# Kernel optimization log

Measured on AMD Instinct MI355X. Metric: run time of the kernel, lower is better.

Reference implementation:

```python
import jax, jax.numpy as jnp
import numpy as np

B, T, DIM, H = 4, 2048, 512, 8
DECAY = 0.9

def setup_inputs():
    key = jax.random.key(0)
    ks = jax.random.split(key, 8)
    s = 1.0 / np.sqrt(DIM)
    def lin(k):
        return jax.random.normal(k, (DIM, DIM), jnp.float32) * s
    return {
        "q": jax.random.normal(ks[0], (B, T, DIM), jnp.float32),
        "k": jax.random.normal(ks[1], (B, T, DIM), jnp.float32),
        "v": jax.random.normal(ks[2], (B, T, DIM), jnp.float32),
        "Wa": lin(ks[3]), "ba": jnp.zeros((DIM,), jnp.float32),
        "Wb": lin(ks[4]), "bb": jnp.zeros((DIM,), jnp.float32),
        "Wg": lin(ks[5]), "bg": jnp.zeros((DIM,), jnp.float32),
        "Wo": lin(ks[6]), "bo": jnp.zeros((DIM,), jnp.float32),
    }

def _linear_scan(a, b):
    # h_t = a_t * h_{t-1} + b_t along time axis=1, via associative scan
    def combine(c1, c2):
        a1, b1 = c1
        a2, b2 = c2
        return a1 * a2, a2 * b1 + b2
    return jax.lax.associative_scan(combine, (a, b), axis=1)[1]

def reference(q, k, v, Wa, ba, Wb, bb, Wg, bg, Wo, bo):
    # --- Mamba-style selective scan on q (no residual) ---
    a = jax.nn.sigmoid(q @ Wa + ba)   # input-dependent decay [B,T,D]
    b = q @ Wb + bb                   # input injection       [B,T,D]
    h = _linear_scan(a, b)            # recurrent state       [B,T,D]
    g = jax.nn.sigmoid(q @ Wg + bg)   # gate
    m_out = (h * g) @ Wo + bo         # [B,T,D]

    # --- RetNet-style decay-weighted linear retention ---
    Dh = DIM // H
    qh = q.reshape(B, T, H, Dh)
    kh = k.reshape(B, T, H, Dh)
    vh = v.reshape(B, T, H, Dh)
    t = jnp.arange(T)
    delta = t[:, None] - t[None, :]           # t - s
    mask = delta >= 0                         # causal
    decay_mat = jnp.where(
        mask,
        jnp.exp(jnp.where(mask, delta, 0).astype(jnp.float32) * np.float32(np.log(DECAY))),
        0.0,
    )                                          # [T,T]
    scores = jnp.einsum('bthd,bshd->bhts', qh, kh) * decay_mat  # [B,H,T,T]
    r_out = jnp.einsum('bhts,bshd->bthd', scores, vh).reshape(B, T, DIM)

    return m_out + r_out
```

## Files before the change

### kernel.cpp

```cpp
#include <hip/hip_runtime.h>
#include <hip/hip_bf16.h>

typedef unsigned short u16;

#define BB 4
#define TT 2048
#define DIM 512
#define NH 8
#define DH 64
#define DECAY 0.9f

#define CC 64
#define NC 32
#define BHN 32

#define CHS 32
#define NSC 64

#define TM 128
#define TN 128
#define BK 64

#define SS 72

typedef __attribute__((ext_vector_type(8))) short bf16x8;
typedef __attribute__((ext_vector_type(4))) float f32x4;

__device__ __forceinline__ u16 f2bfu(float f) {
  union { float f; unsigned int u; } c; c.f = f;
  unsigned int u = c.u + 0x7FFFu + ((c.u >> 16) & 1u);
  return (u16)(u >> 16);
}
__device__ __forceinline__ float bf2f(u16 u) {
  union { unsigned int u; float f; } c; c.u = ((unsigned int)u) << 16;
  return c.f;
}

__device__ __forceinline__ void gl_lds16(const void* g, void* l) {
  __builtin_amdgcn_global_load_lds(
      (const __attribute__((address_space(1))) void*)g,
      (__attribute__((address_space(3))) void*)(unsigned int)(unsigned long long)l,
      16, 0, 0);
}

__device__ __forceinline__ void gemm_tile(
    int nTile, int mTile, const u16* __restrict__ A, const u16* __restrict__ Bt,
    const float* __restrict__ b0, const float* __restrict__ b1,
    const float* __restrict__ b2,
    u16* __restrict__ C0, u16* __restrict__ C1, u16* __restrict__ C2,
    int act_mask, u16* As, u16* Bs, int tid) {
  int wave = tid >> 6, lane = tid & 63;
  int group = (nTile * TN) >> 9;
  const float* bias = (group == 0) ? b0 : (group == 1) ? b1 : b2;
  u16* C = (group == 0) ? C0 : (group == 1) ? C1 : C2;
  int act = (act_mask >> group) & 1;

  int wm = (wave >> 1) * 64, wn = (wave & 1) * 64;
  int rowA = lane & 15, khalf = lane >> 4;

  f32x4 acc[4][4];
#pragma unroll
  for (int i = 0; i < 4; ++i)
#pragma unroll
    for (int j = 0; j < 4; ++j) acc[i][j] = (f32x4){0.f, 0.f, 0.f, 0.f};

  const u16* Abase = A + (size_t)mTile * TM * 512;
  const u16* Bbase = Bt + (size_t)nTile * TN * 512;

  for (int kk = 0; kk < 512; kk += BK) {
#pragma unroll
    for (int i = 0; i < 4; ++i) {
      int o = (wave * 4 + i) * 64 + lane;
      int row = o >> 3, gk = (o & 7) ^ (row & 7);
      gl_lds16(Abase + (size_t)row * 512 + kk + gk * 8, &As[o * 8]);
    }
#pragma unroll
    for (int i = 0; i < 4; ++i) {
      int o = (wave * 4 + i) * 64 + lane;
      int row = o >> 3, gk = (o & 7) ^ (row & 7);
      gl_lds16(Bbase + (size_t)row * 512 + kk + gk * 8, &Bs[o * 8]);
    }
    __syncthreads();
#pragma unroll
    for (int k0 = 0; k0 < 2; ++k0) {
      bf16x8 af[4], bfr[4];
#pragma unroll
      for (int mi = 0; mi < 4; ++mi) {
        int rr = wm + mi * 16 + rowA;
        int gk = k0 * 4 + khalf;
        int o = rr * 8 + (gk ^ (rr & 7));
        af[mi] = *(const bf16x8*)&As[o * 8];
      }
#pragma unroll
      for (int ni = 0; ni < 4; ++ni) {
        int rr = wn + ni * 16 + rowA;
        int gk = k0 * 4 + khalf;
        int o = rr * 8 + (gk ^ (rr & 7));
        bfr[ni] = *(const bf16x8*)&Bs[o * 8];
      }
#pragma unroll
      for (int mi = 0; mi < 4; ++mi)
#pragma unroll
        for (int ni = 0; ni < 4; ++ni)
          acc[mi][ni] = __builtin_amdgcn_mfma_f32_16x16x32_bf16(
              af[mi], bfr[ni], acc[mi][ni], 0, 0, 0);
    }
    __syncthreads();
  }
  int cloc = lane & 15, rq = (lane >> 4) * 4;
#pragma unroll
  for (int mi = 0; mi < 4; ++mi) {
#pragma unroll
    for (int r = 0; r < 4; ++r) {
      int m = mTile * TM + wm + mi * 16 + rq + r;
#pragma unroll
      for (int ni = 0; ni < 4; ++ni) {
        int n = (nTile * TN + wn + ni * 16 + cloc) & 511;
        float vv = acc[mi][ni][r] + bias[n];
        if (act) vv = 1.0f / (1.0f + __expf(-vv));
        C[(size_t)m * 512 + n] = f2bfu(vv);
      }
    }
  }
}

__device__ __forceinline__ void gemm_tile64(
    int nTile, int mTile, const u16* __restrict__ A, const u16* __restrict__ Bt,
    const float* __restrict__ bias, float* __restrict__ C,
    const u16* __restrict__ Radd, u16* As, u16* Bs, int tid) {
  int wave = tid >> 6, lane = tid & 63;
  int wm = wave * 32;
  int rowA = lane & 15, khalf = lane >> 4;

  f32x4 acc[2][4];
#pragma unroll
  for (int i = 0; i < 2; ++i)
#pragma unroll
    for (int j = 0; j < 4; ++j) acc[i][j] = (f32x4){0.f, 0.f, 0.f, 0.f};

  const u16* Abase = A + (size_t)mTile * TM * 512;
  const u16* Bbase = Bt + (size_t)nTile * 64 * 512;

  for (int kk = 0; kk < 512; kk += BK) {
#pragma unroll
    for (int i = 0; i < 4; ++i) {
      int o = (wave * 4 + i) * 64 + lane;
      int row = o >> 3, gk = (o & 7) ^ (row & 7);
      gl_lds16(Abase + (size_t)row * 512 + kk + gk * 8, &As[o * 8]);
    }
#pragma unroll
    for (int i = 0; i < 2; ++i) {
      int o = (wave * 2 + i) * 64 + lane;
      int row = o >> 3, gk = (o & 7) ^ (row & 7);
      gl_lds16(Bbase + (size_t)row * 512 + kk + gk * 8, &Bs[o * 8]);
    }
    __syncthreads();
#pragma unroll
    for (int k0 = 0; k0 < 2; ++k0) {
      bf16x8 af[2], bfr[4];
#pragma unroll
      for (int mi = 0; mi < 2; ++mi) {
        int rr = wm + mi * 16 + rowA;
        int gk = k0 * 4 + khalf;
        int o = rr * 8 + (gk ^ (rr & 7));
        af[mi] = *(const bf16x8*)&As[o * 8];
      }
#pragma unroll
      for (int ni = 0; ni < 4; ++ni) {
        int rr = ni * 16 + rowA;
        int gk = k0 * 4 + khalf;
        int o = rr * 8 + (gk ^ (rr & 7));
        bfr[ni] = *(const bf16x8*)&Bs[o * 8];
      }
#pragma unroll
      for (int mi = 0; mi < 2; ++mi)
#pragma unroll
        for (int ni = 0; ni < 4; ++ni)
          acc[mi][ni] = __builtin_amdgcn_mfma_f32_16x16x32_bf16(
              af[mi], bfr[ni], acc[mi][ni], 0, 0, 0);
    }
    __syncthreads();
  }
  int cloc = lane & 15, rq = (lane >> 4) * 4;
#pragma unroll
  for (int mi = 0; mi < 2; ++mi) {
#pragma unroll
    for (int r = 0; r < 4; ++r) {
      int m = mTile * TM + wm + mi * 16 + rq + r;
#pragma unroll
      for (int ni = 0; ni < 4; ++ni) {
        int n = nTile * 64 + ni * 16 + cloc;
        float vv = acc[mi][ni][r] + bias[n] + bf2f(Radd[(size_t)m * 512 + n]);
        C[(size_t)m * 512 + n] = vv;
      }
    }
  }
}

__global__ __launch_bounds__(256) void k1_prep_retkv(
    const float* __restrict__ q, u16* __restrict__ qbf,
    const float* __restrict__ W0, const float* __restrict__ W1,
    const float* __restrict__ W2, const float* __restrict__ W3,
    u16* __restrict__ Wt,
    const float* __restrict__ k, const float* __restrict__ v,
    u16* __restrict__ KVTb, u16* __restrict__ VTg, u16* __restrict__ kcb) {
  __shared__ __align__(16) u16 smem[2 * 64 * SS];
  __shared__ float t[32][33];
  int bx = blockIdx.x, tid = threadIdx.x;
  if (bx < 1024) {
    int bh = bx & 31, c = bx >> 5;
    int b = bh >> 3, h = bh & 7;
    int wave = tid >> 6, lane = tid & 63;
    u16* VT = smem;
    u16* KT = smem + 64 * SS;
    size_t base = ((size_t)(b * TT + c * CC)) * DIM + h * DH;
    int row = tid >> 2, part = tid & 3, e0 = part * 16;
    float w = __powf(DECAY, (float)(63 - row));
    __align__(16) u16 krow[16];
    {
      const float4* vs = (const float4*)(v + base + (size_t)row * DIM + e0);
      const float4* ks = (const float4*)(k + base + (size_t)row * DIM + e0);
#pragma unroll
      for (int u4 = 0; u4 < 4; ++u4) {
        float4 fv = vs[u4], fk = ks[u4];
        VT[(e0 + u4 * 4 + 0) * SS + row] = f2bfu(fv.x);
        VT[(e0 + u4 * 4 + 1) * SS + row] = f2bfu(fv.y);
        VT[(e0 + u4 * 4 + 2) * SS + row] = f2bfu(fv.z);
        VT[(e0 + u4 * 4 + 3) * SS + row] = f2bfu(fv.w);
        u16 k0s = f2bfu(fk.x * w), k1s = f2bfu(fk.y * w);
        u16 k2s = f2bfu(fk.z * w), k3s = f2bfu(fk.w * w);
        KT[(e0 + u4 * 4 + 0) * SS + row] = k0s;
        KT[(e0 + u4 * 4 + 1) * SS + row] = k1s;
        KT[(e0 + u4 * 4 + 2) * SS + row] = k2s;
        KT[(e0 + u4 * 4 + 3) * SS + row] = k3s;
        krow[u4 * 4 + 0] = k0s; krow[u4 * 4 + 1] = k1s;
        krow[u4 * 4 + 2] = k2s; krow[u4 * 4 + 3] = k3s;
      }
    }
    {
      u16* kdst = kcb + (((size_t)bh * NC + c) * 64 + row) * 64 + e0;
      *(uint4*)kdst = *(const uint4*)&krow[0];
      *(uint4*)(kdst + 8) = *(const uint4*)&krow[8];
    }
    __syncthreads();
    {
      int e = row;
      u16* dst = VTg + ((size_t)bh * 64 + e) * TT + c * 64 + part * 16;
      *(uint4*)dst = *(const uint4*)&VT[e * SS + part * 16];
      *(uint4*)(dst + 8) = *(const uint4*)&VT[e * SS + part * 16 + 8];
    }
    int wm = (wave >> 1) * 32, wn = (wave & 1) * 32;
    int rowA = lane & 15, khalf = lane >> 4;
    f32x4 acc[2][2];
#pragma unroll
    for (int i = 0; i < 2; ++i)
#pragma unroll
      for (int j = 0; j < 2; ++j) acc[i][j] = (f32x4){0.f, 0.f, 0.f, 0.f};
#pragma unroll
    for (int k0 = 0; k0 < 2; ++k0) {
      int gk = k0 * 4 + khalf;
      bf16x8 af[2], bfr[2];
#pragma unroll
      for (int mi = 0; mi < 2; ++mi)
        af[mi] = *(const bf16x8*)&VT[(wm + mi * 16 + rowA) * SS + gk * 8];
#pragma unroll
      for (int ni = 0; ni < 2; ++ni)
        bfr[ni] = *(const bf16x8*)&KT[(wn + ni * 16 + rowA) * SS + gk * 8];
#pragma unroll
      for (int mi = 0; mi < 2; ++mi)
#pragma unroll
        for (int ni = 0; ni < 2; ++ni)
          acc[mi][ni] = __builtin_amdgcn_mfma_f32_16x16x32_bf16(
              af[mi], bfr[ni], acc[mi][ni], 0, 0, 0);
    }
    int cloc = lane & 15, rq = (lane >> 4) * 4;
    u16* o = KVTb + ((size_t)(c * BHN + bh)) * 4096;
#pragma unroll
    for (int mi = 0; mi < 2; ++mi)
#pragma unroll
      for (int r = 0; r < 4; ++r) {
        int e = wm + mi * 16 + rq + r;
#pragma unroll
        for (int ni = 0; ni < 2; ++ni)
          o[e * 64 + (wn + ni * 16 + cloc)] = f2bfu(acc[mi][ni][r]);
      }
  } else if (bx < 2048) {
    int bx2 = bx - 1024;
    int m = bx2 >> 8, rem = bx2 & 255;
    int n0 = (rem & 15) * 32, k0 = (rem >> 4) * 32;
    const float* W = (m == 0) ? W0 : (m == 1) ? W1 : (m == 2) ? W2 : W3;
    int tx = tid & 31, ty = tid >> 5;
#pragma unroll
    for (int r = 0; r < 32; r += 8)
      t[ty + r][tx] = W[(size_t)(k0 + ty + r) * DIM + n0 + tx];
    __syncthreads();
    u16* o = Wt + (size_t)m * DIM * DIM;
#pragma unroll
    for (int r = 0; r < 32; r += 8)
      o[(size_t)(n0 + ty + r) * DIM + k0 + tx] = f2bfu(t[tx][ty + r]);
  } else {
    int i = (bx - 2048) * 256 + tid;
    float4 f = ((const float4*)q)[i];
    ushort4 u;
    u.x = f2bfu(f.x); u.y = f2bfu(f.y); u.z = f2bfu(f.z); u.w = f2bfu(f.w);
    ((ushort4*)qbf)[i] = u;
  }
}

__global__ __launch_bounds__(256) void k2_gemm1_retscan(
    const u16* __restrict__ qbf, const u16* __restrict__ WtAll,
    const float* __restrict__ ba, const float* __restrict__ bb,
    const float* __restrict__ bg,
    u16* __restrict__ Ab16, u16* __restrict__ Bb16, u16* __restrict__ Gb16,
    const u16* __restrict__ KVTb, u16* __restrict__ Ptb) {
  __shared__ __align__(16) u16 smem[TM * BK + TN * BK];
  int bx = blockIdx.x, tid = threadIdx.x;
  if (bx < 768) {
    int r = bx & 7, t6 = bx >> 3;
    int nT = t6 % 12, s = t6 / 12;
    int mT = (s << 3) | r;
    gemm_tile(nT, mT, qbf, WtAll, ba, bb, bg, Ab16, Bb16, Gb16,
              0b101, smem, smem + TM * BK, tid);
  } else {
    int gid = (bx - 768) * 256 + tid;
    int bh = gid >> 12, ed = gid & 4095;
    float carry = 0.f;
    const float dC = __powf(DECAY, (float)CC);
    for (int c = 0; c < NC; ++c) {
      size_t idx = ((size_t)(c * BHN + bh)) * 4096 + ed;
      Ptb[idx] = f2bfu(carry);
      carry = fmaf(dC, carry, bf2f(KVTb[idx]));
    }
  }
}

__global__ __launch_bounds__(256) void k3_retout_part(
    const u16* __restrict__ Ab16, const u16* __restrict__ Bb16,
    float* __restrict__ SA, float* __restrict__ SB,
    const u16* __restrict__ qbf, const u16* __restrict__ kcb,
    const u16* __restrict__ VTg, const u16* __restrict__ Ptb,
    u16* __restrict__ routb) {
  __shared__ __align__(16) u16 Sa[64 * SS];
  __shared__ float dp[66];
  __shared__ float dpi[64];
  int bx = blockIdx.x, tid = threadIdx.x;
  if (bx >= 1024) {
    int bxp = bx - 1024;
    int ci = bxp >> 3, grp = bxp & 7;
    int ch = grp * 256 + tid;
    int bb2 = ch >> 9, d = ch & 511;
    size_t base = ((size_t)bb2 * TT + ci * CHS) * DIM + d;
    float h = 0.f, pA = 1.f;
#pragma unroll
    for (int t = 0; t < CHS; ++t) {
      float av = bf2f(Ab16[base + (size_t)t * DIM]);
      float bv = bf2f(Bb16[base + (size_t)t * DIM]);
      h = fmaf(av, h, bv);
      pA *= av;
    }
    SA[ci * 2048 + ch] = pA;
    SB[ci * 2048 + ch] = h;
    return;
  }
  int bh = bx & 31, c = bx >> 5;
  int b = bh >> 3, h = bh & 7;
  int wave = tid >> 6, lane = tid & 63;
  size_t base = ((size_t)(b * TT + c * CC)) * DIM + h * DH;
  if (tid < 66) dp[tid] = __powf(DECAY, (float)tid);
  if (tid < 64) dpi[tid] = __powf(DECAY, (float)tid - 63.0f);

  int wm = (wave >> 1) * 32, wn = (wave & 1) * 32;
  int rowA = lane & 15, khalf = lane >> 4;

  bf16x8 afq[2][2];
#pragma unroll
  for (int k0 = 0; k0 < 2; ++k0)
#pragma unroll
    for (int mi = 0; mi < 2; ++mi)
      afq[k0][mi] = *(const bf16x8*)(qbf + base +
          (size_t)(wm + mi * 16 + rowA) * 512 + (k0 * 4 + khalf) * 8);
  const u16* kcbase = kcb + ((size_t)bh * NC + c) * 64 * 64;
  bf16x8 bfk[2][2];
#pragma unroll
  for (int k0 = 0; k0 < 2; ++k0)
#pragma unroll
    for (int ni = 0; ni < 2; ++ni)
      bfk[k0][ni] = *(const bf16x8*)(kcbase +
          (size_t)(wn + ni * 16 + rowA) * 64 + (k0 * 4 + khalf) * 8);

  f32x4 accS[2][2];
#pragma unroll
  for (int i = 0; i < 2; ++i)
#pragma unroll
    for (int j = 0; j < 2; ++j) accS[i][j] = (f32x4){0.f, 0.f, 0.f, 0.f};
#pragma unroll
  for (int k0 = 0; k0 < 2; ++k0)
#pragma unroll
    for (int mi = 0; mi < 2; ++mi)
#pragma unroll
      for (int ni = 0; ni < 2; ++ni)
        accS[mi][ni] = __builtin_amdgcn_mfma_f32_16x16x32_bf16(
            afq[k0][mi], bfk[k0][ni], accS[mi][ni], 0, 0, 0);
  __syncthreads();

  int cloc = lane & 15, rq = (lane >> 4) * 4;
#pragma unroll
  for (int mi = 0; mi < 2; ++mi)
#pragma unroll
    for (int ni = 0; ni < 2; ++ni)
#pragma unroll
      for (int r = 0; r < 4; ++r) {
        int i = wm + mi * 16 + rq + r;
        int j = wn + ni * 16 + cloc;
        float sv = (j <= i) ? accS[mi][ni][r] * dpi[i] : 0.f;
        Sa[i * SS + j] = f2bfu(sv);
      }
#pragma unroll
  for (int mi = 0; mi < 2; ++mi) {
    float s = dp[wm + mi * 16 + rowA + 1];
#pragma unroll
    for (int k0 = 0; k0 < 2; ++k0) {
      bf16x8 t = afq[k0][mi];
#pragma unroll
      for (int u = 0; u < 8; ++u)
        t[u] = (short)f2bfu(bf2f((u16)t[u]) * s);
      afq[k0][mi] = t;
    }
  }
  __syncthreads();

  f32x4 accO[2][2];
#pragma unroll
  for (int i = 0; i < 2; ++i)
#pragma unroll
    for (int j = 0; j < 2; ++j) accO[i][j] = (f32x4){0.f, 0.f, 0.f, 0.f};
#pragma unroll
  for (int k0 = 0; k0 < 4; ++k0) {
    bf16x8 af[2], bfv[2];
#pragma unroll
    for (int mi = 0; mi < 2; ++mi) {
      if (k0 < 2)
        af[mi] = *(const bf16x8*)&Sa[(wm + mi * 16 + rowA) * SS +
                                     (k0 * 4 + khalf) * 8];
      else
        af[mi] = afq[k0 - 2][mi];
    }
#pragma unroll
    for (int ni = 0; ni < 2; ++ni) {
      int e = wn + ni * 16 + rowA;
      if (k0 < 2)
        bfv[ni] = *(const bf16x8*)(VTg + ((size_t)bh * 64 + e) * TT + c * 64 +
                                   (k0 * 4 + khalf) * 8);
      else
        bfv[ni] = *(const bf16x8*)(Ptb + ((size_t)(c * BHN + bh)) * 4096 +
                                   e * 64 + ((k0 - 2) * 4 + khalf) * 8);
    }
#pragma unroll
    for (int mi = 0; mi < 2; ++mi)
#pragma unroll
      for (int ni = 0; ni < 2; ++ni)
        accO[mi][ni] = __builtin_amdgcn_mfma_f32_16x16x32_bf16(
            af[mi], bfv[ni], accO[mi][ni], 0, 0, 0);
  }
#pragma unroll
  for (int mi = 0; mi < 2; ++mi)
#pragma unroll
    for (int r = 0; r < 4; ++r) {
      int i = wm + mi * 16 + rq + r;
#pragma unroll
      for (int ni = 0; ni < 2; ++ni) {
        int e = wn + ni * 16 + cloc;
        routb[base + (size_t)i * 512 + e] = f2bfu(accO[mi][ni][r]);
      }
    }
}

__global__ __launch_bounds__(256) void k4_apply(
    const u16* __restrict__ Ab16, const u16* __restrict__ Bb16,
    const u16* __restrict__ g, const float* __restrict__ SA,
    const float* __restrict__ SB, u16* __restrict__ hg) {
  int bx = blockIdx.x, tid = threadIdx.x;
  int ci = bx >> 3, grp = bx & 7;
  int ch = grp * 256 + tid;
  int bb = ch >> 9, d = ch & 511;
  float carry = 0.f;
  for (int p = 0; p < ci; ++p)
    carry = fmaf(SA[p * 2048 + ch], carry, SB[p * 2048 + ch]);
  size_t base = ((size_t)bb * TT + ci * CHS) * DIM + d;
  float h = carry;
#pragma unroll
  for (int t = 0; t < CHS; ++t) {
    size_t idx = base + (size_t)t * DIM;
    h = fmaf(bf2f(Ab16[idx]), h, bf2f(Bb16[idx]));
    hg[idx] = f2bfu(h * bf2f(g[idx]));
  }
}

__global__ __launch_bounds__(256) void k5_gemm2(
    const u16* __restrict__ hgbf, const u16* __restrict__ Wto,
    const float* __restrict__ bo, float* __restrict__ out,
    const u16* __restrict__ routb) {
  __shared__ __align__(16) u16 smem[TM * BK + 64 * BK];
  int bx = blockIdx.x;
  int r = bx & 7, t6 = bx >> 3;
  int nT = t6 & 7, s = t6 >> 3;
  int mT = (s << 3) | r;
  gemm_tile64(nT, mT, hgbf, Wto, bo, out, routb,
              smem, smem + TM * BK, threadIdx.x);
}

extern "C" void kernel_launch(void* const* d_in, const int* in_sizes, int n_in,
                              void* d_out, int out_size, void* d_ws, size_t ws_size,
                              hipStream_t stream) {
  const float* q  = (const float*)d_in[0];
  const float* k  = (const float*)d_in[1];
  const float* v  = (const float*)d_in[2];
  const float* Wa = (const float*)d_in[3];
  const float* ba = (const float*)d_in[4];
  const float* Wb = (const float*)d_in[5];
  const float* bb = (const float*)d_in[6];
  const float* Wg = (const float*)d_in[7];
  const float* bg = (const float*)d_in[8];
  const float* Wo = (const float*)d_in[9];
  const float* bo = (const float*)d_in[10];
  float* out = (float*)d_out;
  float* ws = (float*)d_ws;

  const size_t NEL = (size_t)BB * TT * DIM;
  float* SA = ws;
  float* SB = SA + NSC * 2048;
  u16* up = (u16*)(SB + NSC * 2048);
  u16* Ab16  = up;  up += NEL;
  u16* Bb16  = up;  up += NEL;
  u16* Gb16  = up;  up += NEL;
  u16* qbf   = up;  up += NEL;
  u16* hgbf  = up;  up += NEL;
  u16* WtAll = up;  up += 4 * DIM * DIM;
  u16* KVTb  = up;  up += (size_t)NC * BHN * 4096;
  u16* Ptb   = up;  up += (size_t)NC * BHN * 4096;
  u16* VTg   = up;  up += (size_t)BHN * 64 * TT;
  u16* routb = up;  up += NEL;
  u16* kcb   = up;  up += (size_t)BHN * NC * 64 * 64;

  k1_prep_retkv<<<6144, 256, 0, stream>>>(q, qbf, Wa, Wb, Wg, Wo, WtAll,
                                          k, v, KVTb, VTg, kcb);

  k2_gemm1_retscan<<<1280, 256, 0, stream>>>(qbf, WtAll, ba, bb, bg,
                                             Ab16, Bb16, Gb16, KVTb, Ptb);

  k3_retout_part<<<1536, 256, 0, stream>>>(Ab16, Bb16, SA, SB,
                                           qbf, kcb, VTg, Ptb, routb);

  k4_apply<<<512, 256, 0, stream>>>(Ab16, Bb16, Gb16, SA, SB, hgbf);

  k5_gemm2<<<512, 256, 0, stream>>>(hgbf, WtAll + 3 * DIM * DIM,
                                    bo, out, routb);
}
```

Before: 174.4 us.

## Fuse stages k2-k5 into one persistent cooperative kernel with grid syncs

Replaces four separate kernel launches (GEMM1+retention scan, retention output+chunk partials, scan apply, output GEMM) with a single cooperative kernel of 512 blocks that loops over work units and separates the stages with grid-wide syncs. The aim is to remove launch gaps and tail effects between the stages. In exchange, each block handles several units serially and occupancy is fixed at two blocks per CU. Load balance also changes, since some blocks do two GEMM tiles while others do two scan units. A fallback to the old launches is kept in case the cooperative launch fails.

```diff
diff --git a/kernel.cpp b/kernel.cpp
--- a/kernel.cpp
+++ b/kernel.cpp
@@ -1,5 +1,8 @@
 #include <hip/hip_runtime.h>
 #include <hip/hip_bf16.h>
+#include <hip/hip_cooperative_groups.h>
+
+namespace cg = cooperative_groups;
 
 typedef unsigned short u16;
 
@@ -195,6 +198,178 @@
       }
     }
   }
+}
+
+__device__ __forceinline__ void dev_retscan(int unit, int tid,
+    const u16* __restrict__ KVTb, u16* __restrict__ Ptb) {
+  int gid = unit * 256 + tid;
+  int bh = gid >> 12, ed = gid & 4095;
+  float carry = 0.f;
+  const float dC = __powf(DECAY, (float)CC);
+#pragma unroll
+  for (int c = 0; c < NC; ++c) {
+    size_t idx = ((size_t)(c * BHN + bh)) * 4096 + ed;
+    Ptb[idx] = f2bfu(carry);
+    carry = fmaf(dC, carry, bf2f(KVTb[idx]));
+  }
+}
+
+__device__ __forceinline__ void dev_part(int unit, int tid,
+    const u16* __restrict__ Ab16, const u16* __restrict__ Bb16,
+    float* __restrict__ SA, float* __restrict__ SB) {
+  int ci = unit >> 3, grp = unit & 7;
+  int ch = grp * 256 + tid;
+  int bb2 = ch >> 9, d = ch & 511;
+  size_t base = ((size_t)bb2 * TT + ci * CHS) * DIM + d;
+  float h = 0.f, pA = 1.f;
+#pragma unroll
+  for (int t = 0; t < CHS; ++t) {
+    float av = bf2f(Ab16[base + (size_t)t * DIM]);
+    float bv = bf2f(Bb16[base + (size_t)t * DIM]);
+    h = fmaf(av, h, bv);
+    pA *= av;
+  }
+  SA[ci * 2048 + ch] = pA;
+  SB[ci * 2048 + ch] = h;
+}
+
+__device__ __forceinline__ void dev_apply(int unit, int tid,
+    const u16* __restrict__ Ab16, const u16* __restrict__ Bb16,
+    const u16* __restrict__ g, const float* __restrict__ SA,
+    const float* __restrict__ SB, u16* __restrict__ hg) {
+  int ci = unit >> 3, grp = unit & 7;
+  int ch = grp * 256 + tid;
+  int bb = ch >> 9, d = ch & 511;
+  float carry = 0.f;
+  for (int p = 0; p < ci; ++p)
+    carry = fmaf(SA[p * 2048 + ch], carry, SB[p * 2048 + ch]);
+  size_t base = ((size_t)bb * TT + ci * CHS) * DIM + d;
+  float h = carry;
+#pragma unroll
+  for (int t = 0; t < CHS; ++t) {
+    size_t idx = base + (size_t)t * DIM;
+    h = fmaf(bf2f(Ab16[idx]), h, bf2f(Bb16[idx]));
+    hg[idx] = f2bfu(h * bf2f(g[idx]));
+  }
+}
+
+__device__ __forceinline__ void dev_retout(int unit, int tid,
+    u16* Sa, float* dp, float* dpi,
+    const u16* __restrict__ qbf, const u16* __restrict__ kcb,
+    const u16* __restrict__ VTg, const u16* __restrict__ Ptb,
+    u16* __restrict__ routb) {
+  __syncthreads();
+  int bh = unit & 31, c = unit >> 5;
+  int b = bh >> 3, h = bh & 7;
+  int wave = tid >> 6, lane = tid & 63;
+  size_t base = ((size_t)(b * TT + c * CC)) * DIM + h * DH;
+  if (tid < 66) dp[tid] = __powf(DECAY, (float)tid);
+  if (tid < 64) dpi[tid] = __powf(DECAY, (float)tid - 63.0f);
+
+  int wm = (wave >> 1) * 32, wn = (wave & 1) * 32;
+  int rowA = lane & 15, khalf = lane >> 4;
+
+  bf16x8 afq[2][2];
+#pragma unroll
+  for (int k0 = 0; k0 < 2; ++k0)
+#pragma unroll
+    for (int mi = 0; mi < 2; ++mi)
+      afq[k0][mi] = *(const bf16x8*)(qbf + base +
+          (size_t)(wm + mi * 16 + rowA) * 512 + (k0 * 4 + khalf) * 8);
+  const u16* kcbase = kcb + ((size_t)bh * NC + c) * 64 * 64;
+  bf16x8 bfk[2][2];
+#pragma unroll
+  for (int k0 = 0; k0 < 2; ++k0)
+#pragma unroll
+    for (int ni = 0; ni < 2; ++ni)
+      bfk[k0][ni] = *(const bf16x8*)(kcbase +
+          (size_t)(wn + ni * 16 + rowA) * 64 + (k0 * 4 + khalf) * 8);
+
+  f32x4 accS[2][2];
+#pragma unroll
+  for (int i = 0; i < 2; ++i)
+#pragma unroll
+    for (int j = 0; j < 2; ++j) accS[i][j] = (f32x4){0.f, 0.f, 0.f, 0.f};
+#pragma unroll
+  for (int k0 = 0; k0 < 2; ++k0)
+#pragma unroll
+    for (int mi = 0; mi < 2; ++mi)
+#pragma unroll
+      for (int ni = 0; ni < 2; ++ni)
+        accS[mi][ni] = __builtin_amdgcn_mfma_f32_16x16x32_bf16(
+            afq[k0][mi], bfk[k0][ni], accS[mi][ni], 0, 0, 0);
+  __syncthreads();
+
+  int cloc = lane & 15, rq = (lane >> 4) * 4;
+#pragma unroll
+  for (int mi = 0; mi < 2; ++mi)
+#pragma unroll
+    for (int ni = 0; ni < 2; ++ni)
+#pragma unroll
+      for (int r = 0; r < 4; ++r) {
+        int i = wm + mi * 16 + rq + r;
+        int j = wn + ni * 16 + cloc;
+        float sv = (j <= i) ? accS[mi][ni][r] * dpi[i] : 0.f;
+        Sa[i * SS + j] = f2bfu(sv);
+      }
+#pragma unroll
+  for (int mi = 0; mi < 2; ++mi) {
+    float s = dp[wm + mi * 16 + rowA + 1];
+#pragma unroll
+    for (int k0 = 0; k0 < 2; ++k0) {
+      bf16x8 t = afq[k0][mi];
+#pragma unroll
+      for (int u = 0; u < 8; ++u)
+        t[u] = (short)f2bfu(bf2f((u16)t[u]) * s);
+      afq[k0][mi] = t;
+    }
+  }
+  __syncthreads();
+
+  f32x4 accO[2][2];
+#pragma unroll
+  for (int i = 0; i < 2; ++i)
+#pragma unroll
+    for (int j = 0; j < 2; ++j) accO[i][j] = (f32x4){0.f, 0.f, 0.f, 0.f};
+#pragma unroll
+  for (int k0 = 0; k0 < 4; ++k0) {
+    bf16x8 af[2], bfv[2];
+#pragma unroll
+    for (int mi = 0; mi < 2; ++mi) {
+      if (k0 < 2)
+        af[mi] = *(const bf16x8*)&Sa[(wm + mi * 16 + rowA) * SS +
+                                     (k0 * 4 + khalf) * 8];
+      else
+        af[mi] = afq[k0 - 2][mi];
+    }
+#pragma unroll
+    for (int ni = 0; ni < 2; ++ni) {
+      int e = wn + ni * 16 + rowA;
+      if (k0 < 2)
+        bfv[ni] = *(const bf16x8*)(VTg + ((size_t)bh * 64 + e) * TT + c * 64 +
+                                   (k0 * 4 + khalf) * 8);
+      else
+        bfv[ni] = *(const bf16x8*)(Ptb + ((size_t)(c * BHN + bh)) * 4096 +
+                                   e * 64 + ((k0 - 2) * 4 + khalf) * 8);
+    }
+#pragma unroll
+    for (int mi = 0; mi < 2; ++mi)
+#pragma unroll
+      for (int ni = 0; ni < 2; ++ni)
+        accO[mi][ni] = __builtin_amdgcn_mfma_f32_16x16x32_bf16(
+            af[mi], bfv[ni], accO[mi][ni], 0, 0, 0);
+  }
+#pragma unroll
+  for (int mi = 0; mi < 2; ++mi)
+#pragma unroll
+    for (int r = 0; r < 4; ++r) {
+      int i = wm + mi * 16 + rq + r;
+#pragma unroll
+      for (int ni = 0; ni < 2; ++ni) {
+        int e = wn + ni * 16 + cloc;
+        routb[base + (size_t)i * 512 + e] = f2bfu(accO[mi][ni][r]);
+      }
+    }
 }
 
 __global__ __launch_bounds__(256) void k1_prep_retkv(
@@ -307,6 +482,54 @@
   }
 }
 
+__global__ __launch_bounds__(256, 2) void k2to5_fused(
+    const u16* __restrict__ qbf, const u16* __restrict__ WtAll,
+    const float* __restrict__ ba, const float* __restrict__ bb,
+    const float* __restrict__ bg,
+    u16* __restrict__ Ab16, u16* __restrict__ Bb16, u16* __restrict__ Gb16,
+    const u16* __restrict__ KVTb, u16* __restrict__ Ptb,
+    float* __restrict__ SA, float* __restrict__ SB,
+    const u16* __restrict__ kcb, const u16* __restrict__ VTg,
+    u16* __restrict__ routb, u16* __restrict__ hgbf,
+    const float* __restrict__ bo, float* __restrict__ out) {
+  __shared__ __align__(16) u16 smem[TM * BK + TN * BK];
+  int b = blockIdx.x, tid = threadIdx.x;
+  {
+    int r = b & 7, t6 = b >> 3;
+    int nT = t6 % 12, s = t6 / 12;
+    gemm_tile(nT, (s << 3) | r, qbf, WtAll, ba, bb, bg, Ab16, Bb16, Gb16,
+              0b101, smem, smem + TM * BK, tid);
+  }
+  if (b < 256) {
+    int t1 = b + 512;
+    int r = t1 & 7, t6 = t1 >> 3;
+    int nT = t6 % 12, s = t6 / 12;
+    gemm_tile(nT, (s << 3) | r, qbf, WtAll, ba, bb, bg, Ab16, Bb16, Gb16,
+              0b101, smem, smem + TM * BK, tid);
+  } else {
+    dev_retscan((b - 256) * 2, tid, KVTb, Ptb);
+    dev_retscan((b - 256) * 2 + 1, tid, KVTb, Ptb);
+  }
+  cg::this_grid().sync();
+  {
+    u16* Sa = smem;
+    float* dp = (float*)(smem + 4608);
+    float* dpi = dp + 66;
+    dev_retout(b, tid, Sa, dp, dpi, qbf, kcb, VTg, Ptb, routb);
+    dev_retout(b + 512, tid, Sa, dp, dpi, qbf, kcb, VTg, Ptb, routb);
+    dev_part(b, tid, Ab16, Bb16, SA, SB);
+  }
+  cg::this_grid().sync();
+  dev_apply(b, tid, Ab16, Bb16, Gb16, SA, SB, hgbf);
+  cg::this_grid().sync();
+  {
+    int r = b & 7, t6 = b >> 3;
+    int nT = t6 & 7, s = t6 >> 3;
+    gemm_tile64(nT, (s << 3) | r, hgbf, WtAll + 3 * DIM * DIM, bo, out, routb,
+                smem, smem + TM * BK, tid);
+  }
+}
+
 __global__ __launch_bounds__(256) void k2_gemm1_retscan(
     const u16* __restrict__ qbf, const u16* __restrict__ WtAll,
     const float* __restrict__ ba, const float* __restrict__ bb,
@@ -318,19 +541,10 @@
   if (bx < 768) {
     int r = bx & 7, t6 = bx >> 3;
     int nT = t6 % 12, s = t6 / 12;
-    int mT = (s << 3) | r;
-    gemm_tile(nT, mT, qbf, WtAll, ba, bb, bg, Ab16, Bb16, Gb16,
+    gemm_tile(nT, (s << 3) | r, qbf, WtAll, ba, bb, bg, Ab16, Bb16, Gb16,
               0b101, smem, smem + TM * BK, tid);
   } else {
-    int gid = (bx - 768) * 256 + tid;
-    int bh = gid >> 12, ed = gid & 4095;
-    float carry = 0.f;
-    const float dC = __powf(DECAY, (float)CC);
-    for (int c = 0; c < NC; ++c) {
-      size_t idx = ((size_t)(c * BHN + bh)) * 4096 + ed;
-      Ptb[idx] = f2bfu(carry);
-      carry = fmaf(dC, carry, bf2f(KVTb[idx]));
-    }
+    dev_retscan(bx - 768, tid, KVTb, Ptb);
   }
 }
 
@@ -345,155 +559,17 @@
   __shared__ float dpi[64];
   int bx = blockIdx.x, tid = threadIdx.x;
   if (bx >= 1024) {
-    int bxp = bx - 1024;
-    int ci = bxp >> 3, grp = bxp & 7;
-    int ch = grp * 256 + tid;
-    int bb2 = ch >> 9, d = ch & 511;
-    size_t base = ((size_t)bb2 * TT + ci * CHS) * DIM + d;
-    float h = 0.f, pA = 1.f;
-#pragma unroll
-    for (int t = 0; t < CHS; ++t) {
-      float av = bf2f(Ab16[base + (size_t)t * DIM]);
-      float bv = bf2f(Bb16[base + (size_t)t * DIM]);
-      h = fmaf(av, h, bv);
-      pA *= av;
-    }
-    SA[ci * 2048 + ch] = pA;
-    SB[ci * 2048 + ch] = h;
+    dev_part(bx - 1024, tid, Ab16, Bb16, SA, SB);
     return;
   }
-  int bh = bx & 31, c = bx >> 5;
-  int b = bh >> 3, h = bh & 7;
-  int wave = tid >> 6, lane = tid & 63;
-  size_t base = ((size_t)(b * TT + c * CC)) * DIM + h * DH;
-  if (tid < 66) dp[tid] = __powf(DECAY, (float)tid);
-  if (tid < 64) dpi[tid] = __powf(DECAY, (float)tid - 63.0f);
-
-  int wm = (wave >> 1) * 32, wn = (wave & 1) * 32;
-  int rowA = lane & 15, khalf = lane >> 4;
-
-  bf16x8 afq[2][2];
-#pragma unroll
-  for (int k0 = 0; k0 < 2; ++k0)
-#pragma unroll
-    for (int mi = 0; mi < 2; ++mi)
-      afq[k0][mi] = *(const bf16x8*)(qbf + base +
-          (size_t)(wm + mi * 16 + rowA) * 512 + (k0 * 4 + khalf) * 8);
-  const u16* kcbase = kcb + ((size_t)bh * NC + c) * 64 * 64;
-  bf16x8 bfk[2][2];
-#pragma unroll
-  for (int k0 = 0; k0 < 2; ++k0)
-#pragma unroll
-    for (int ni = 0; ni < 2; ++ni)
-      bfk[k0][ni] = *(const bf16x8*)(kcbase +
-          (size_t)(wn + ni * 16 + rowA) * 64 + (k0 * 4 + khalf) * 8);
-
-  f32x4 accS[2][2];
-#pragma unroll
-  for (int i = 0; i < 2; ++i)
-#pragma unroll
-    for (int j = 0; j < 2; ++j) accS[i][j] = (f32x4){0.f, 0.f, 0.f, 0.f};
-#pragma unroll
-  for (int k0 = 0; k0 < 2; ++k0)
-#pragma unroll
-    for (int mi = 0; mi < 2; ++mi)
-#pragma unroll
-      for (int ni = 0; ni < 2; ++ni)
-        accS[mi][ni] = __builtin_amdgcn_mfma_f32_16x16x32_bf16(
-            afq[k0][mi], bfk[k0][ni], accS[mi][ni], 0, 0, 0);
-  __syncthreads();
-
-  int cloc = lane & 15, rq = (lane >> 4) * 4;
-#pragma unroll
-  for (int mi = 0; mi < 2; ++mi)
-#pragma unroll
-    for (int ni = 0; ni < 2; ++ni)
-#pragma unroll
-      for (int r = 0; r < 4; ++r) {
-        int i = wm + mi * 16 + rq + r;
-        int j = wn + ni * 16 + cloc;
-        float sv = (j <= i) ? accS[mi][ni][r] * dpi[i] : 0.f;
-        Sa[i * SS + j] = f2bfu(sv);
-      }
-#pragma unroll
-  for (int mi = 0; mi < 2; ++mi) {
-    float s = dp[wm + mi * 16 + rowA + 1];
-#pragma unroll
-    for (int k0 = 0; k0 < 2; ++k0) {
-      bf16x8 t = afq[k0][mi];
-#pragma unroll
-      for (int u = 0; u < 8; ++u)
-        t[u] = (short)f2bfu(bf2f((u16)t[u]) * s);
-      afq[k0][mi] = t;
-    }
-  }
-  __syncthreads();
-
-  f32x4 accO[2][2];
-#pragma unroll
-  for (int i = 0; i < 2; ++i)
-#pragma unroll
-    for (int j = 0; j < 2; ++j) accO[i][j] = (f32x4){0.f, 0.f, 0.f, 0.f};
-#pragma unroll
-  for (int k0 = 0; k0 < 4; ++k0) {
-    bf16x8 af[2], bfv[2];
-#pragma unroll
-    for (int mi = 0; mi < 2; ++mi) {
-      if (k0 < 2)
-        af[mi] = *(const bf16x8*)&Sa[(wm + mi * 16 + rowA) * SS +
-                                     (k0 * 4 + khalf) * 8];
-      else
-        af[mi] = afq[k0 - 2][mi];
-    }
-#pragma unroll
-    for (int ni = 0; ni < 2; ++ni) {
-      int e = wn + ni * 16 + rowA;
-      if (k0 < 2)
-        bfv[ni] = *(const bf16x8*)(VTg + ((size_t)bh * 64 + e) * TT + c * 64 +
-                                   (k0 * 4 + khalf) * 8);
-      else
-        bfv[ni] = *(const bf16x8*)(Ptb + ((size_t)(c * BHN + bh)) * 4096 +
-                                   e * 64 + ((k0 - 2) * 4 + khalf) * 8);
-    }
-#pragma unroll
-    for (int mi = 0; mi < 2; ++mi)
-#pragma unroll
-      for (int ni = 0; ni < 2; ++ni)
-        accO[mi][ni] = __builtin_amdgcn_mfma_f32_16x16x32_bf16(
-            af[mi], bfv[ni], accO[mi][ni], 0, 0, 0);
-  }
-#pragma unroll
-  for (int mi = 0; mi < 2; ++mi)
-#pragma unroll
-    for (int r = 0; r < 4; ++r) {
-      int i = wm + mi * 16 + rq + r;
-#pragma unroll
-      for (int ni = 0; ni < 2; ++ni) {
-        int e = wn + ni * 16 + cloc;
-        routb[base + (size_t)i * 512 + e] = f2bfu(accO[mi][ni][r]);
-      }
-    }
+  dev_retout(bx, tid, Sa, dp, dpi, qbf, kcb, VTg, Ptb, routb);
 }
 
 __global__ __launch_bounds__(256) void k4_apply(
     const u16* __restrict__ Ab16, const u16* __restrict__ Bb16,
     const u16* __restrict__ g, const float* __restrict__ SA,
     const float* __restrict__ SB, u16* __restrict__ hg) {
-  int bx = blockIdx.x, tid = threadIdx.x;
-  int ci = bx >> 3, grp = bx & 7;
-  int ch = grp * 256 + tid;
-  int bb = ch >> 9, d = ch & 511;
-  float carry = 0.f;
-  for (int p = 0; p < ci; ++p)
-    carry = fmaf(SA[p * 2048 + ch], carry, SB[p * 2048 + ch]);
-  size_t base = ((size_t)bb * TT + ci * CHS) * DIM + d;
-  float h = carry;
-#pragma unroll
-  for (int t = 0; t < CHS; ++t) {
-    size_t idx = base + (size_t)t * DIM;
-    h = fmaf(bf2f(Ab16[idx]), h, bf2f(Bb16[idx]));
-    hg[idx] = f2bfu(h * bf2f(g[idx]));
-  }
+  dev_apply(blockIdx.x, threadIdx.x, Ab16, Bb16, g, SA, SB, hg);
 }
 
 __global__ __launch_bounds__(256) void k5_gemm2(
@@ -504,8 +580,7 @@
   int bx = blockIdx.x;
   int r = bx & 7, t6 = bx >> 3;
   int nT = t6 & 7, s = t6 >> 3;
-  int mT = (s << 3) | r;
-  gemm_tile64(nT, mT, hgbf, Wto, bo, out, routb,
+  gemm_tile64(nT, (s << 3) | r, hgbf, Wto, bo, out, routb,
               smem, smem + TM * BK, threadIdx.x);
 }
 
@@ -545,14 +620,23 @@
   k1_prep_retkv<<<6144, 256, 0, stream>>>(q, qbf, Wa, Wb, Wg, Wo, WtAll,
                                           k, v, KVTb, VTg, kcb);
 
-  k2_gemm1_retscan<<<1280, 256, 0, stream>>>(qbf, WtAll, ba, bb, bg,
-                                             Ab16, Bb16, Gb16, KVTb, Ptb);
-
-  k3_retout_part<<<1536, 256, 0, stream>>>(Ab16, Bb16, SA, SB,
-                                           qbf, kcb, VTg, Ptb, routb);
-
-  k4_apply<<<512, 256, 0, stream>>>(Ab16, Bb16, Gb16, SA, SB, hgbf);
-
-  k5_gemm2<<<512, 256, 0, stream>>>(hgbf, WtAll + 3 * DIM * DIM,
-                                    bo, out, routb);
-}
+  const u16* qbf_c = qbf; const u16* Wt_c = WtAll;
+  const u16* KVTb_c = KVTb; const u16* kcb_c = kcb; const u16* VTg_c = VTg;
+  void* kargs[] = {
+      (void*)&qbf_c, (void*)&Wt_c, (void*)&ba, (void*)&bb, (void*)&bg,
+      (void*)&Ab16, (void*)&Bb16, (void*)&Gb16, (void*)&KVTb_c, (void*)&Ptb,
+      (void*)&SA, (void*)&SB, (void*)&kcb_c, (void*)&VTg_c, (void*)&routb,
+      (void*)&hgbf, (void*)&bo, (void*)&out};
+  hipError_t e = hipLaunchCooperativeKernel((const void*)k2to5_fused,
+                                            dim3(512), dim3(256), kargs, 0,
+                                            stream);
+  if (e != hipSuccess) {
+    k2_gemm1_retscan<<<1280, 256, 0, stream>>>(qbf, WtAll, ba, bb, bg,
+                                               Ab16, Bb16, Gb16, KVTb, Ptb);
+    k3_retout_part<<<1536, 256, 0, stream>>>(Ab16, Bb16, SA, SB,
+                                             qbf, kcb, VTg, Ptb, routb);
+    k4_apply<<<512, 256, 0, stream>>>(Ab16, Bb16, Gb16, SA, SB, hgbf);
+    k5_gemm2<<<512, 256, 0, stream>>>(hgbf, WtAll + 3 * DIM * DIM,
+                                      bo, out, routb);
+  }
+}
```

New measurement: 400.3 us. +129.5%, slower.

## Fuse chunked selective scan into single-pass decoupled look-back in retention kernel

Applied to the files above, without the earlier changes.

Replaces the two-kernel chunked scan (per-chunk summaries followed by a serial carry apply kernel) with a single-pass decoupled look-back scan. Each block publishes its aggregate and inclusive prefix through 64-bit atomic flags that are reset to a sentinel in the prep kernel, and the blocks scan blocks are placed first in the retention kernel. It keeps A and B in registers so they are read once instead of twice, and it removes one launch and the O(ci) carry loop. In exchange it relies on blocks being scheduled in index order for forward progress, and it spin-waits with sleeps. The q-to-bf16 conversion is also widened to two float4 per thread.

```diff
diff --git a/kernel.cpp b/kernel.cpp
--- a/kernel.cpp
+++ b/kernel.cpp
@@ -2,6 +2,7 @@
 #include <hip/hip_bf16.h>
 
 typedef unsigned short u16;
+typedef unsigned long long u64;
 
 #define BB 4
 #define TT 2048
@@ -22,6 +23,8 @@
 #define BK 64
 
 #define SS 72
+
+#define SENT 0xFFFFFFFFFFFFFFFFull
 
 typedef __attribute__((ext_vector_type(8))) short bf16x8;
 typedef __attribute__((ext_vector_type(4))) float f32x4;
@@ -197,13 +200,85 @@
   }
 }
 
+__device__ __forceinline__ void dev_retscan(int unit, int tid,
+    const u16* __restrict__ KVTb, u16* __restrict__ Ptb) {
+  int gid = unit * 256 + tid;
+  int bh = gid >> 12, ed = gid & 4095;
+  float carry = 0.f;
+  const float dC = __powf(DECAY, (float)CC);
+#pragma unroll
+  for (int c = 0; c < NC; ++c) {
+    size_t idx = ((size_t)(c * BHN + bh)) * 4096 + ed;
+    Ptb[idx] = f2bfu(carry);
+    carry = fmaf(dC, carry, bf2f(KVTb[idx]));
+  }
+}
+
+__device__ __forceinline__ void dev_scan_fused(int bxu, int tid,
+    const u16* __restrict__ Ab16, const u16* __restrict__ Bb16,
+    const u16* __restrict__ g, u64* __restrict__ Agg, u64* __restrict__ Inc,
+    u16* __restrict__ hg) {
+  int ci = bxu >> 3, grp = bxu & 7;
+  int ch = grp * 256 + tid;
+  int bb = ch >> 9, d = ch & 511;
+  size_t base = ((size_t)bb * TT + ci * CHS) * DIM + d;
+  float a[CHS], b[CHS];
+  float pA = 1.f, hloc = 0.f;
+#pragma unroll
+  for (int t = 0; t < CHS; ++t) {
+    a[t] = bf2f(Ab16[base + (size_t)t * DIM]);
+    b[t] = bf2f(Bb16[base + (size_t)t * DIM]);
+    hloc = fmaf(a[t], hloc, b[t]);
+    pA *= a[t];
+  }
+  union PK { u64 u; float2 f; } pk;
+  float carry = 0.f;
+  if (ci == 0) {
+    pk.f.x = 1.0f; pk.f.y = hloc;
+    __hip_atomic_store(&Inc[ch], pk.u, __ATOMIC_RELEASE,
+                       __HIP_MEMORY_SCOPE_AGENT);
+  } else {
+    pk.f.x = pA; pk.f.y = hloc;
+    __hip_atomic_store(&Agg[(size_t)ci * 2048 + ch], pk.u, __ATOMIC_RELEASE,
+                       __HIP_MEMORY_SCOPE_AGENT);
+    float sA = 1.f, sB = 0.f;
+    int p = ci - 1;
+    for (;;) {
+      union PK q;
+      q.u = __hip_atomic_load(&Inc[(size_t)p * 2048 + ch], __ATOMIC_ACQUIRE,
+                              __HIP_MEMORY_SCOPE_AGENT);
+      if (q.u != SENT) { carry = fmaf(sA, q.f.y, sB); break; }
+      q.u = __hip_atomic_load(&Agg[(size_t)p * 2048 + ch], __ATOMIC_ACQUIRE,
+                              __HIP_MEMORY_SCOPE_AGENT);
+      if (q.u != SENT) {
+        sB = fmaf(sA, q.f.y, sB);
+        sA = sA * q.f.x;
+        --p;
+      } else {
+        __builtin_amdgcn_s_sleep(1);
+      }
+    }
+    pk.f.x = 1.0f; pk.f.y = fmaf(pA, carry, hloc);
+    __hip_atomic_store(&Inc[(size_t)ci * 2048 + ch], pk.u, __ATOMIC_RELEASE,
+                       __HIP_MEMORY_SCOPE_AGENT);
+  }
+  float h = carry;
+#pragma unroll
+  for (int t = 0; t < CHS; ++t) {
+    size_t idx = base + (size_t)t * DIM;
+    h = fmaf(a[t], h, b[t]);
+    hg[idx] = f2bfu(h * bf2f(g[idx]));
+  }
+}
+
 __global__ __launch_bounds__(256) void k1_prep_retkv(
     const float* __restrict__ q, u16* __restrict__ qbf,
     const float* __restrict__ W0, const float* __restrict__ W1,
     const float* __restrict__ W2, const float* __restrict__ W3,
     u16* __restrict__ Wt,
     const float* __restrict__ k, const float* __restrict__ v,
-    u16* __restrict__ KVTb, u16* __restrict__ VTg, u16* __restrict__ kcb) {
+    u16* __restrict__ KVTb, u16* __restrict__ VTg, u16* __restrict__ kcb,
+    u64* __restrict__ Flags) {
   __shared__ __align__(16) u16 smem[2 * 64 * SS];
   __shared__ float t[32][33];
   int bx = blockIdx.x, tid = threadIdx.x;
@@ -298,12 +373,20 @@
 #pragma unroll
     for (int r = 0; r < 32; r += 8)
       o[(size_t)(n0 + ty + r) * DIM + k0 + tx] = f2bfu(t[tx][ty + r]);
+  } else if (bx < 4096) {
+    int i0 = ((bx - 2048) * 256 + tid) * 2;
+#pragma unroll
+    for (int u2 = 0; u2 < 2; ++u2) {
+      float4 f = ((const float4*)q)[i0 + u2];
+      ushort4 u;
+      u.x = f2bfu(f.x); u.y = f2bfu(f.y); u.z = f2bfu(f.z); u.w = f2bfu(f.w);
+      ((ushort4*)qbf)[i0 + u2] = u;
+    }
   } else {
-    int i = (bx - 2048) * 256 + tid;
-    float4 f = ((const float4*)q)[i];
-    ushort4 u;
-    u.x = f2bfu(f.x); u.y = f2bfu(f.y); u.z = f2bfu(f.z); u.w = f2bfu(f.w);
-    ((ushort4*)qbf)[i] = u;
+    int j = (bx - 4096) * 256 + tid;
+    uint4 s = make_uint4(0xFFFFFFFFu, 0xFFFFFFFFu, 0xFFFFFFFFu, 0xFFFFFFFFu);
+    uint4* p = (uint4*)(Flags + (size_t)j * 8);
+    p[0] = s; p[1] = s;
   }
 }
 
@@ -322,21 +405,14 @@
     gemm_tile(nT, mT, qbf, WtAll, ba, bb, bg, Ab16, Bb16, Gb16,
               0b101, smem, smem + TM * BK, tid);
   } else {
-    int gid = (bx - 768) * 256 + tid;
-    int bh = gid >> 12, ed = gid & 4095;
-    float carry = 0.f;
-    const float dC = __powf(DECAY, (float)CC);
-    for (int c = 0; c < NC; ++c) {
-      size_t idx = ((size_t)(c * BHN + bh)) * 4096 + ed;
-      Ptb[idx] = f2bfu(carry);
-      carry = fmaf(dC, carry, bf2f(KVTb[idx]));
-    }
-  }
-}
-
-__global__ __launch_bounds__(256) void k3_retout_part(
+    dev_retscan(bx - 768, tid, KVTb, Ptb);
+  }
+}
+
+__global__ __launch_bounds__(256) void k3_scan_retout(
     const u16* __restrict__ Ab16, const u16* __restrict__ Bb16,
-    float* __restrict__ SA, float* __restrict__ SB,
+    const u16* __restrict__ Gb16, u64* __restrict__ Agg, u64* __restrict__ Inc,
+    u16* __restrict__ hg,
     const u16* __restrict__ qbf, const u16* __restrict__ kcb,
     const u16* __restrict__ VTg, const u16* __restrict__ Ptb,
     u16* __restrict__ routb) {
@@ -344,25 +420,12 @@
   __shared__ float dp[66];
   __shared__ float dpi[64];
   int bx = blockIdx.x, tid = threadIdx.x;
-  if (bx >= 1024) {
-    int bxp = bx - 1024;
-    int ci = bxp >> 3, grp = bxp & 7;
-    int ch = grp * 256 + tid;
-    int bb2 = ch >> 9, d = ch & 511;
-    size_t base = ((size_t)bb2 * TT + ci * CHS) * DIM + d;
-    float h = 0.f, pA = 1.f;
-#pragma unroll
-    for (int t = 0; t < CHS; ++t) {
-      float av = bf2f(Ab16[base + (size_t)t * DIM]);
-      float bv = bf2f(Bb16[base + (size_t)t * DIM]);
-      h = fmaf(av, h, bv);
-      pA *= av;
-    }
-    SA[ci * 2048 + ch] = pA;
-    SB[ci * 2048 + ch] = h;
+  if (bx < 512) {
+    dev_scan_fused(bx, tid, Ab16, Bb16, Gb16, Agg, Inc, hg);
     return;
   }
-  int bh = bx & 31, c = bx >> 5;
+  int idx2 = bx - 512;
+  int bh = idx2 & 31, c = idx2 >> 5;
   int b = bh >> 3, h = bh & 7;
   int wave = tid >> 6, lane = tid & 63;
   size_t base = ((size_t)(b * TT + c * CC)) * DIM + h * DH;
@@ -473,27 +536,6 @@
         routb[base + (size_t)i * 512 + e] = f2bfu(accO[mi][ni][r]);
       }
     }
-}
-
-__global__ __launch_bounds__(256) void k4_apply(
-    const u16* __restrict__ Ab16, const u16* __restrict__ Bb16,
-    const u16* __restrict__ g, const float* __restrict__ SA,
-    const float* __restrict__ SB, u16* __restrict__ hg) {
-  int bx = blockIdx.x, tid = threadIdx.x;
-  int ci = bx >> 3, grp = bx & 7;
-  int ch = grp * 256 + tid;
-  int bb = ch >> 9, d = ch & 511;
-  float carry = 0.f;
-  for (int p = 0; p < ci; ++p)
-    carry = fmaf(SA[p * 2048 + ch], carry, SB[p * 2048 + ch]);
-  size_t base = ((size_t)bb * TT + ci * CHS) * DIM + d;
-  float h = carry;
-#pragma unroll
-  for (int t = 0; t < CHS; ++t) {
-    size_t idx = base + (size_t)t * DIM;
-    h = fmaf(bf2f(Ab16[idx]), h, bf2f(Bb16[idx]));
-    hg[idx] = f2bfu(h * bf2f(g[idx]));
-  }
 }
 
 __global__ __launch_bounds__(256) void k5_gemm2(
@@ -524,12 +566,11 @@
   const float* Wo = (const float*)d_in[9];
   const float* bo = (const float*)d_in[10];
   float* out = (float*)d_out;
-  float* ws = (float*)d_ws;
 
   const size_t NEL = (size_t)BB * TT * DIM;
-  float* SA = ws;
-  float* SB = SA + NSC * 2048;
-  u16* up = (u16*)(SB + NSC * 2048);
+  u64* Agg = (u64*)d_ws;
+  u64* Inc = Agg + (size_t)NSC * 2048;
+  u16* up = (u16*)(Inc + (size_t)NSC * 2048);
   u16* Ab16  = up;  up += NEL;
   u16* Bb16  = up;  up += NEL;
   u16* Gb16  = up;  up += NEL;
@@ -542,16 +583,14 @@
   u16* routb = up;  up += NEL;
   u16* kcb   = up;  up += (size_t)BHN * NC * 64 * 64;
 
-  k1_prep_retkv<<<6144, 256, 0, stream>>>(q, qbf, Wa, Wb, Wg, Wo, WtAll,
-                                          k, v, KVTb, VTg, kcb);
+  k1_prep_retkv<<<4224, 256, 0, stream>>>(q, qbf, Wa, Wb, Wg, Wo, WtAll,
+                                          k, v, KVTb, VTg, kcb, Agg);
 
   k2_gemm1_retscan<<<1280, 256, 0, stream>>>(qbf, WtAll, ba, bb, bg,
                                              Ab16, Bb16, Gb16, KVTb, Ptb);
 
-  k3_retout_part<<<1536, 256, 0, stream>>>(Ab16, Bb16, SA, SB,
+  k3_scan_retout<<<1536, 256, 0, stream>>>(Ab16, Bb16, Gb16, Agg, Inc, hgbf,
                                            qbf, kcb, VTg, Ptb, routb);
-
-  k4_apply<<<512, 256, 0, stream>>>(Ab16, Bb16, Gb16, SA, SB, hgbf);
 
   k5_gemm2<<<512, 256, 0, stream>>>(hgbf, WtAll + 3 * DIM * DIM,
                                     bo, out, routb);
```

New measurement: 439.2 us. 2.52x slower.
